# Kernel optimization log

Hardware: AMD Instinct MI355X
Metric: run time of the kernel (lower is better)

Reference implementation:

```python
import math
import jax, jax.numpy as jnp
import numpy as np

NUM_HEADS = 8
K_CRITICAL = 0.05
K_SKIP = 0.10


def setup_inputs() -> dict:
    key = jax.random.key(0)
    ks = jax.random.split(key, 10)
    B, T, D = 1, 2048, 512
    s = 1.0 / math.sqrt(D)
    return {
        'x': jax.random.normal(ks[0], (B, T, D), jnp.float32),
        'wq': jax.random.normal(ks[1], (D, D), jnp.float32) * s,
        'bq': jax.random.normal(ks[2], (D,), jnp.float32) * s,
        'wk': jax.random.normal(ks[3], (D, D), jnp.float32) * s,
        'bk': jax.random.normal(ks[4], (D,), jnp.float32) * s,
        'wv': jax.random.normal(ks[5], (D, D), jnp.float32) * s,
        'bv': jax.random.normal(ks[6], (D,), jnp.float32) * s,
        'wo': jax.random.normal(ks[7], (D, D), jnp.float32) * s,
        'bo': jax.random.normal(ks[8], (D,), jnp.float32) * s,
    }


def _phi(t):
    # elu(t) + 1 -> positive feature map for linear attention
    return jax.nn.elu(t) + 1.0


def reference(x, wq, bq, wk, bk, wv, bv, wo, bo):
    B, T, D = x.shape
    H = NUM_HEADS
    hd = D // H

    # projections (torch nn.Linear: y = x @ W.T + b), split heads -> [B,H,T,hd]
    q = (x @ wq.T + bq).reshape(B, T, H, hd).transpose(0, 2, 1, 3)
    k = (x @ wk.T + bk).reshape(B, T, H, hd).transpose(0, 2, 1, 3)
    v = (x @ wv.T + bv).reshape(B, T, H, hd).transpose(0, 2, 1, 3)

    # full attention scores [B,H,T,T]
    scores = jnp.einsum('bhqd,bhkd->bhqk', q, k) / math.sqrt(hd)

    # per-query quantile thresholds (linear interpolation, like torch.quantile)
    crit_th = jnp.quantile(scores, 1.0 - K_CRITICAL, axis=-1, keepdims=True)
    skip_th = jnp.quantile(scores, K_SKIP, axis=-1, keepdims=True)
    crit_mask = scores > crit_th
    skip_mask = scores < skip_th
    marginal_mask = jnp.logical_not(crit_mask | skip_mask)

    # critical path: softmax over top-k_critical entries only
    crit_scores = jnp.where(crit_mask, scores, -jnp.inf)
    crit_attn = jax.nn.softmax(crit_scores, axis=-1)
    crit_attn = jnp.where(skip_mask, 0.0, crit_attn)
    crit_out = jnp.einsum('bhqk,bhkd->bhqd', crit_attn, v)

    # marginal path: causal (cumulative) linear attention
    q_f = _phi(q)
    k_f = _phi(k)
    kv_cum = jnp.cumsum(k_f[..., :, None] * v[..., None, :], axis=2)  # [B,H,T,hd,hd]
    k_cum = jnp.cumsum(k_f, axis=2)                                   # [B,H,T,hd]
    lin_num = jnp.einsum('bhtd,bhtde->bhte', q_f, kv_cum)             # [B,H,T,hd]
    lin_den = jnp.clip(jnp.sum(q_f * k_cum, axis=-1, keepdims=True), 1e-6, None)
    marginal_active = jnp.mean(marginal_mask.astype(scores.dtype), axis=-1, keepdims=True)
    lin_out = (lin_num / lin_den) * marginal_active

    out = (crit_out + lin_out).transpose(0, 2, 1, 3).reshape(B, T, D)
    out = out @ wo.T + bo  # dropout is identity in eval mode
    return out
```

## Files before the change

kernel.cpp:

```cpp
#include <hip/hip_runtime.h>
#include <math.h>

#define T_SEQ 2048
#define D_MODEL 512
#define H_HEADS 8
#define HD 64
#define NCH 32
#define CSZ 64
#define CAP 192

__device__ __forceinline__ unsigned f2k(float f) {
    unsigned u = __float_as_uint(f);
    return (u & 0x80000000u) ? ~u : (u | 0x80000000u);
}
__device__ __forceinline__ float k2f(unsigned k) {
    unsigned u = (k & 0x80000000u) ? (k & 0x7fffffffu) : ~k;
    return __uint_as_float(u);
}

__device__ __forceinline__ void locate_rank(unsigned rr, unsigned e0,
    const unsigned cc[4], int lane, unsigned& sel_bin, unsigned& sel_nb, unsigned& sel_cnt)
{
    unsigned e1 = e0 + cc[0], e2 = e1 + cc[1], e3 = e2 + cc[2];
    int bin = -1; unsigned nb = 0u, ct = 0u;
    if (rr >= e0 && rr < e1)              { bin = lane * 4 + 0; nb = e0; ct = cc[0]; }
    else if (rr >= e1 && rr < e2)         { bin = lane * 4 + 1; nb = e1; ct = cc[1]; }
    else if (rr >= e2 && rr < e3)         { bin = lane * 4 + 2; nb = e2; ct = cc[2]; }
    else if (rr >= e3 && rr < e3 + cc[3]) { bin = lane * 4 + 3; nb = e3; ct = cc[3]; }
    unsigned long long bal = __ballot(bin >= 0);
    int src = __ffsll((unsigned long long)bal) - 1;
    sel_bin = (unsigned)__shfl(bin, src);
    sel_nb  = (unsigned)__shfl((int)nb, src);
    sel_cnt = (unsigned)__shfl((int)ct, src);
}

__global__ __launch_bounds__(256) void proj_qkv_kernel(
    const float* __restrict__ x,
    const float* __restrict__ wq, const float* __restrict__ bq,
    const float* __restrict__ wk, const float* __restrict__ bk,
    const float* __restrict__ wv, const float* __restrict__ bv,
    float* __restrict__ qh, float* __restrict__ kh, float* __restrict__ vh,
    float* __restrict__ qf, float* __restrict__ kf)
{
    const int which = blockIdx.z;
    const float* W    = (which == 0) ? wq : (which == 1) ? wk : wv;
    const float* bias = (which == 0) ? bq : (which == 1) ? bk : bv;
    float* outh = (which == 0) ? qh : (which == 1) ? kh : vh;
    float* outf = (which == 0) ? qf : (which == 1) ? kf : nullptr;

    __shared__ float As[32][68];
    __shared__ float Bs[32][68];
    const int tid = threadIdx.x;
    const int m0 = blockIdx.x * 64;
    const int n0 = blockIdx.y * 64;
    const int rb = (tid >> 4) * 4;
    const int cb = (tid & 15) * 4;

    float acc[4][4] = {};
    for (int k0 = 0; k0 < D_MODEL; k0 += 32) {
        for (int l = 0; l < 2; ++l) {
            int p = tid + l * 256;
            int row = p >> 3;
            int c4 = (p & 7) * 4;
            float4 av = *(const float4*)(x + (size_t)(m0 + row) * D_MODEL + k0 + c4);
            As[c4 + 0][row] = av.x; As[c4 + 1][row] = av.y;
            As[c4 + 2][row] = av.z; As[c4 + 3][row] = av.w;
            float4 wv4 = *(const float4*)(W + (size_t)(n0 + row) * D_MODEL + k0 + c4);
            Bs[c4 + 0][row] = wv4.x; Bs[c4 + 1][row] = wv4.y;
            Bs[c4 + 2][row] = wv4.z; Bs[c4 + 3][row] = wv4.w;
        }
        __syncthreads();
        #pragma unroll
        for (int kk = 0; kk < 32; ++kk) {
            float4 ar = *(const float4*)&As[kk][rb];
            float4 br = *(const float4*)&Bs[kk][cb];
            float arr[4] = {ar.x, ar.y, ar.z, ar.w};
            float brr[4] = {br.x, br.y, br.z, br.w};
            #pragma unroll
            for (int i = 0; i < 4; ++i)
                #pragma unroll
                for (int j = 0; j < 4; ++j)
                    acc[i][j] = fmaf(arr[i], brr[j], acc[i][j]);
        }
        __syncthreads();
    }
    #pragma unroll
    for (int i = 0; i < 4; ++i) {
        int m = m0 + rb + i;
        #pragma unroll
        for (int j = 0; j < 4; ++j) {
            int n = n0 + cb + j;
            float v = acc[i][j] + bias[n];
            int h = n >> 6, d = n & 63;
            size_t idx = ((size_t)(h * T_SEQ) + m) * HD + d;
            outh[idx] = v;
            if (outf) outf[idx] = (v > 0.f) ? (v + 1.f) : expf(v);
        }
    }
}

__global__ __launch_bounds__(256) void out_proj_kernel(
    const float* __restrict__ att, const float* __restrict__ wo,
    const float* __restrict__ bo, float* __restrict__ out)
{
    __shared__ float As[32][68];
    __shared__ float Bs[32][68];
    const int tid = threadIdx.x;
    const int m0 = blockIdx.x * 64;
    const int n0 = blockIdx.y * 64;
    const int rb = (tid >> 4) * 4;
    const int cb = (tid & 15) * 4;

    float acc[4][4] = {};
    for (int k0 = 0; k0 < D_MODEL; k0 += 32) {
        for (int l = 0; l < 2; ++l) {
            int p = tid + l * 256;
            int row = p >> 3;
            int c4 = (p & 7) * 4;
            float4 av = *(const float4*)(att + (size_t)(m0 + row) * D_MODEL + k0 + c4);
            As[c4 + 0][row] = av.x; As[c4 + 1][row] = av.y;
            As[c4 + 2][row] = av.z; As[c4 + 3][row] = av.w;
            float4 wv4 = *(const float4*)(wo + (size_t)(n0 + row) * D_MODEL + k0 + c4);
            Bs[c4 + 0][row] = wv4.x; Bs[c4 + 1][row] = wv4.y;
            Bs[c4 + 2][row] = wv4.z; Bs[c4 + 3][row] = wv4.w;
        }
        __syncthreads();
        #pragma unroll
        for (int kk = 0; kk < 32; ++kk) {
            float4 ar = *(const float4*)&As[kk][rb];
            float4 br = *(const float4*)&Bs[kk][cb];
            float arr[4] = {ar.x, ar.y, ar.z, ar.w};
            float brr[4] = {br.x, br.y, br.z, br.w};
            #pragma unroll
            for (int i = 0; i < 4; ++i)
                #pragma unroll
                for (int j = 0; j < 4; ++j)
                    acc[i][j] = fmaf(arr[i], brr[j], acc[i][j]);
        }
        __syncthreads();
    }
    #pragma unroll
    for (int i = 0; i < 4; ++i) {
        int m = m0 + rb + i;
        #pragma unroll
        for (int j = 0; j < 4; ++j) {
            int n = n0 + cb + j;
            out[(size_t)m * D_MODEL + n] = acc[i][j] + bo[n];
        }
    }
}

__global__ __launch_bounds__(256) void qk_gemm_kernel(
    const float* __restrict__ qh, const float* __restrict__ kh, float* __restrict__ S)
{
    __shared__ float As[64][132];
    __shared__ float Bs[64][68];
    const int tid = threadIdx.x;
    const int n0 = blockIdx.x * 64;
    const int m0 = blockIdx.y * 128;
    const int h  = blockIdx.z;
    const float* qb = qh + (size_t)h * T_SEQ * HD;
    const float* kb = kh + (size_t)h * T_SEQ * HD;

    #pragma unroll
    for (int l = 0; l < 8; ++l) {
        int p = tid + l * 256;
        int row = p >> 4, c4 = (p & 15) * 4;
        float4 a = *(const float4*)(qb + (size_t)(m0 + row) * HD + c4);
        As[c4 + 0][row] = a.x; As[c4 + 1][row] = a.y;
        As[c4 + 2][row] = a.z; As[c4 + 3][row] = a.w;
    }
    #pragma unroll
    for (int l = 0; l < 4; ++l) {
        int p = tid + l * 256;
        int row = p >> 4, c4 = (p & 15) * 4;
        float4 b = *(const float4*)(kb + (size_t)(n0 + row) * HD + c4);
        Bs[c4 + 0][row] = b.x; Bs[c4 + 1][row] = b.y;
        Bs[c4 + 2][row] = b.z; Bs[c4 + 3][row] = b.w;
    }
    __syncthreads();

    const int rb = (tid >> 4) * 8;
    const int cb = (tid & 15) * 4;
    float acc[8][4] = {};
    #pragma unroll 8
    for (int kk = 0; kk < HD; ++kk) {
        float4 a0 = *(const float4*)&As[kk][rb];
        float4 a1 = *(const float4*)&As[kk][rb + 4];
        float4 br = *(const float4*)&Bs[kk][cb];
        float arr[8] = {a0.x, a0.y, a0.z, a0.w, a1.x, a1.y, a1.z, a1.w};
        float brr[4] = {br.x, br.y, br.z, br.w};
        #pragma unroll
        for (int i = 0; i < 8; ++i)
            #pragma unroll
            for (int j = 0; j < 4; ++j)
                acc[i][j] = fmaf(arr[i], brr[j], acc[i][j]);
    }
    #pragma unroll
    for (int i = 0; i < 8; ++i) {
        float4 o;
        o.x = acc[i][0] * 0.125f; o.y = acc[i][1] * 0.125f;
        o.z = acc[i][2] * 0.125f; o.w = acc[i][3] * 0.125f;
        *(float4*)(S + ((size_t)h * T_SEQ + m0 + rb + i) * T_SEQ + n0 + cb) = o;
    }
}

__global__ __launch_bounds__(256) void select_kernel(
    const float* __restrict__ S, const float* __restrict__ vh,
    float* __restrict__ att, float* __restrict__ marg)
{
    const int h = blockIdx.y;
    const int r = threadIdx.x >> 6;
    const int lane = threadIdx.x & 63;
    const int t = blockIdx.x * 4 + r;
    __shared__ unsigned hists[4][2][256];

    const float* srow = S + ((size_t)h * T_SEQ + t) * T_SEQ;
    unsigned kr[32];
    unsigned mx = 0u;
    #pragma unroll
    for (int u = 0; u < 8; ++u) {
        float4 f = *(const float4*)(srow + (size_t)(lane + u * 64) * 4);
        kr[u * 4 + 0] = f2k(f.x); kr[u * 4 + 1] = f2k(f.y);
        kr[u * 4 + 2] = f2k(f.z); kr[u * 4 + 3] = f2k(f.w);
        mx = max(mx, max(max(kr[u * 4 + 0], kr[u * 4 + 1]), max(kr[u * 4 + 2], kr[u * 4 + 3])));
    }
    #pragma unroll
    for (int off = 32; off > 0; off >>= 1)
        mx = max(mx, (unsigned)__shfl_xor(mx, off));

    const unsigned rankv[2] = {204u, 1944u};
    unsigned pfx[2], base[2] = {0u, 0u}, fct[2] = {0u, 0u};
    bool res[2] = {false, false};
    unsigned rsh[2] = {0u, 0u};

    {
        uint4 z4 = make_uint4(0u, 0u, 0u, 0u);
        uint4* hv = (uint4*)hists[r];
        hv[lane * 2 + 0] = z4; hv[lane * 2 + 1] = z4;
        #pragma unroll
        for (int u = 0; u < 32; ++u)
            atomicAdd(&hists[r][0][kr[u] >> 24], 1u);
        uint4 a = ((const uint4*)hists[r][0])[lane];
        unsigned cc[4] = {a.x, a.y, a.z, a.w};
        unsigned lsum = cc[0] + cc[1] + cc[2] + cc[3];
        unsigned incl = lsum;
        #pragma unroll
        for (int off = 1; off < 64; off <<= 1) {
            unsigned tv = __shfl_up(incl, off);
            if (lane >= off) incl += tv;
        }
        unsigned e0 = incl - lsum;
        #pragma unroll
        for (int g = 0; g < 2; ++g) {
            unsigned bin, nb, ct;
            locate_rank(rankv[g], e0, cc, lane, bin, nb, ct);
            pfx[g] = bin; base[g] = nb; fct[g] = ct;
            if (ct == 1u) { res[g] = true; rsh[g] = 24u; }
        }
    }

    for (int p = 1; p < 4; ++p) {
        if (res[0] && res[1]) break;
        const int sh = 24 - 8 * p;
        const bool a0 = !res[0], a1 = !res[1];
        const bool dup = a0 && a1 && (pfx[0] == pfx[1]);
        uint4 z4 = make_uint4(0u, 0u, 0u, 0u);
        uint4* hv = (uint4*)hists[r];
        hv[lane * 2 + 0] = z4; hv[lane * 2 + 1] = z4;
        #pragma unroll
        for (int u = 0; u < 32; ++u) {
            unsigned k = kr[u];
            unsigned hi = k >> (sh + 8);
            unsigned bin = (k >> sh) & 255u;
            if (a0 && hi == pfx[0]) atomicAdd(&hists[r][0][bin], 1u);
            if (a1 && !dup && hi == pfx[1]) atomicAdd(&hists[r][1][bin], 1u);
        }
        unsigned cc0[4], e00 = 0u;
        if (a0 || dup) {
            uint4 a = ((const uint4*)hists[r][0])[lane];
            cc0[0] = a.x; cc0[1] = a.y; cc0[2] = a.z; cc0[3] = a.w;
            unsigned lsum = cc0[0] + cc0[1] + cc0[2] + cc0[3];
            unsigned incl = lsum;
            #pragma unroll
            for (int off = 1; off < 64; off <<= 1) {
                unsigned tv = __shfl_up(incl, off);
                if (lane >= off) incl += tv;
            }
            e00 = incl - lsum;
        }
        if (a0) {
            unsigned bin, nb, ct;
            locate_rank(rankv[0] - base[0], e00, cc0, lane, bin, nb, ct);
            pfx[0] = (pfx[0] << 8) | bin; base[0] += nb; fct[0] = ct;
            if (ct == 1u && p < 3) { res[0] = true; rsh[0] = (unsigned)sh; }
        }
        if (a1) {
            unsigned bin, nb, ct;
            if (dup) {
                locate_rank(rankv[1] - base[1], e00, cc0, lane, bin, nb, ct);
            } else {
                uint4 b = ((const uint4*)hists[r][1])[lane];
                unsigned cc1[4] = {b.x, b.y, b.z, b.w};
                unsigned lsum = cc1[0] + cc1[1] + cc1[2] + cc1[3];
                unsigned incl = lsum;
                #pragma unroll
                for (int off = 1; off < 64; off <<= 1) {
                    unsigned tv = __shfl_up(incl, off);
                    if (lane >= off) incl += tv;
                }
                unsigned e10 = incl - lsum;
                locate_rank(rankv[1] - base[1], e10, cc1, lane, bin, nb, ct);
            }
            pfx[1] = (pfx[1] << 8) | bin; base[1] += nb; fct[1] = ct;
            if (ct == 1u && p < 3) { res[1] = true; rsh[1] = (unsigned)sh; }
        }
    }

    unsigned kth0, kth1;
    if (res[0] || res[1]) {
        unsigned m0v = 0xffffffffu, m1v = 0xffffffffu;
        #pragma unroll
        for (int u = 0; u < 32; ++u) {
            unsigned k = kr[u];
            if (res[0] && (k >> rsh[0]) == pfx[0]) m0v = min(m0v, k);
            if (res[1] && (k >> rsh[1]) == pfx[1]) m1v = min(m1v, k);
        }
        #pragma unroll
        for (int off = 32; off > 0; off >>= 1) {
            m0v = min(m0v, (unsigned)__shfl_xor(m0v, off));
            m1v = min(m1v, (unsigned)__shfl_xor(m1v, off));
        }
        kth0 = res[0] ? m0v : pfx[0];
        kth1 = res[1] ? m1v : pfx[1];
    } else {
        kth0 = pfx[0]; kth1 = pfx[1];
    }
    (void)kth0;

    const unsigned cle0 = base[0] + fct[0];
    const unsigned scnt = (cle0 > 205u) ? base[0] : cle0;
    const float m = k2f(mx);

    float2* list = (float2*)hists[r];
    float z = 0.f;
    unsigned bcnt = 0;
    const unsigned long long pm = (lane == 0) ? 0ull : (~0ull >> (64 - lane));
    #pragma unroll
    for (int u8 = 0; u8 < 8; ++u8) {
        #pragma unroll
        for (int q = 0; q < 4; ++q) {
            unsigned k = kr[u8 * 4 + q];
            bool crit = k > kth1;
            unsigned long long bal = __ballot(crit);
            if (crit) {
                float sv = k2f(k);
                float w = __expf(sv - m);
                z += w;
                unsigned pos = bcnt + (unsigned)__popcll(bal & pm);
                if (pos < CAP) {
                    unsigned j = (unsigned)(4 * lane + 256 * u8 + q);
                    list[pos] = make_float2(w, __uint_as_float(j));
                }
            }
            bcnt += (unsigned)__popcll(bal);
        }
    }
    #pragma unroll
    for (int off = 32; off > 0; off >>= 1)
        z += __shfl_xor(z, off);
    const float invz = (z > 0.f) ? (1.f / z) : 0.f;

    const float* vb = vh + (size_t)h * T_SEQ * HD;
    const int cnt = (int)min(bcnt, (unsigned)CAP);
    float acc = 0.f;
    int i = 0;
    for (; i + 4 <= cnt; i += 4) {
        float2 e0 = list[i], e1 = list[i + 1], e2 = list[i + 2], e3 = list[i + 3];
        acc = fmaf(e0.x, vb[(size_t)__float_as_uint(e0.y) * HD + lane], acc);
        acc = fmaf(e1.x, vb[(size_t)__float_as_uint(e1.y) * HD + lane], acc);
        acc = fmaf(e2.x, vb[(size_t)__float_as_uint(e2.y) * HD + lane], acc);
        acc = fmaf(e3.x, vb[(size_t)__float_as_uint(e3.y) * HD + lane], acc);
    }
    for (; i < cnt; ++i) {
        float2 e = list[i];
        acc = fmaf(e.x, vb[(size_t)__float_as_uint(e.y) * HD + lane], acc);
    }
    att[(size_t)t * D_MODEL + h * HD + lane] = acc * invz;
    if (lane == 0) {
        unsigned mc = (unsigned)T_SEQ - bcnt - scnt;
        marg[(size_t)h * T_SEQ + t] = (float)mc * (1.f / (float)T_SEQ);
    }
}

__global__ __launch_bounds__(256) void chunk_sums_kernel(
    const float* __restrict__ kf, const float* __restrict__ vh,
    float* __restrict__ Ac, float* __restrict__ bc)
{
    const int c = blockIdx.x, h = blockIdx.y;
    const int tid = threadIdx.x;
    __shared__ float kfl[CSZ][HD];
    __shared__ float vl[CSZ][HD];
    const size_t base = ((size_t)h * T_SEQ + c * CSZ) * HD;

    for (int l = 0; l < 4; ++l) {
        int p = tid + l * 256;
        int row = p >> 4, c4 = (p & 15) * 4;
        *(float4*)&kfl[row][c4] = *(const float4*)(kf + base + (size_t)row * HD + c4);
        *(float4*)&vl[row][c4]  = *(const float4*)(vh + base + (size_t)row * HD + c4);
    }
    __syncthreads();

    const int d = tid >> 2, e0 = (tid & 3) * 16;
    float acc[16] = {};
    for (int u = 0; u < CSZ; ++u) {
        float a = kfl[u][d];
        #pragma unroll
        for (int i = 0; i < 16; ++i) acc[i] = fmaf(a, vl[u][e0 + i], acc[i]);
    }
    float* Adst = Ac + (((size_t)(h * NCH + c) * HD + d) * HD + e0);
    #pragma unroll
    for (int i = 0; i < 16; ++i) Adst[i] = acc[i];

    if (tid < HD) {
        float sum = 0.f;
        for (int u = 0; u < CSZ; ++u) sum += kfl[u][tid];
        bc[(size_t)(h * NCH + c) * HD + tid] = sum;
    }
}

__global__ __launch_bounds__(256) void prefix_kernel(
    const float* __restrict__ Ac, const float* __restrict__ bc,
    float* __restrict__ Sx, float* __restrict__ sx)
{
    const int h = blockIdx.x;
    const int tid = threadIdx.x;
    float run[16];
    #pragma unroll
    for (int i = 0; i < 16; ++i) run[i] = 0.f;
    for (int c = 0; c < NCH; ++c) {
        const float* a = Ac + (size_t)(h * NCH + c) * 4096;
        float* sdst = Sx + (size_t)(h * NCH + c) * 4096;
        #pragma unroll
        for (int i = 0; i < 16; ++i) {
            int idx = tid + i * 256;
            sdst[idx] = run[i];
            run[i] += a[idx];
        }
    }
    if (tid < HD) {
        float rb = 0.f;
        for (int c = 0; c < NCH; ++c) {
            sx[(size_t)(h * NCH + c) * HD + tid] = rb;
            rb += bc[(size_t)(h * NCH + c) * HD + tid];
        }
    }
}

__global__ __launch_bounds__(256) void lin_combine_kernel(
    const float* __restrict__ qf, const float* __restrict__ kf, const float* __restrict__ vh,
    const float* __restrict__ Sx, const float* __restrict__ sx,
    const float* __restrict__ marg, float* __restrict__ att)
{
    const int c = blockIdx.x, h = blockIdx.y;
    const int tid = threadIdx.x;
    __shared__ float Qs[CSZ][65];
    __shared__ float Ks[CSZ][65];
    __shared__ float P[CSZ][66];
    __shared__ float svv[HD];
    __shared__ float coef[CSZ];

    const size_t base = ((size_t)h * T_SEQ + c * CSZ) * HD;
    for (int l = 0; l < 4; ++l) {
        int p = tid + l * 256;
        int row = p >> 4, c4 = (p & 15) * 4;
        *(float4*)&Qs[row][c4] = *(const float4*)(qf + base + (size_t)row * HD + c4);
        *(float4*)&Ks[row][c4] = *(const float4*)(kf + base + (size_t)row * HD + c4);
    }
    if (tid < HD) svv[tid] = sx[(size_t)(h * NCH + c) * HD + tid];
    __syncthreads();

    {
        const int tq = tid >> 2, u0 = (tid & 3) * 16;
        float pr[16];
        #pragma unroll
        for (int i = 0; i < 16; ++i) pr[i] = 0.f;
        for (int d = 0; d < HD; ++d) {
            float qv = Qs[tq][d];
            #pragma unroll
            for (int i = 0; i < 16; ++i) pr[i] = fmaf(qv, Ks[u0 + i][d], pr[i]);
        }
        #pragma unroll
        for (int i = 0; i < 16; ++i) P[tq][u0 + i] = (u0 + i <= tq) ? pr[i] : 0.f;
    }
    __syncthreads();

    if (tid < CSZ) {
        const int tq = tid;
        float den = 0.f;
        for (int d = 0; d < HD; ++d) den += Qs[tq][d] * svv[d];
        for (int u = 0; u <= tq; ++u) den += P[tq][u];
        den = fmaxf(den, 1e-6f);
        coef[tq] = marg[(size_t)h * T_SEQ + c * CSZ + tq] / den;
    }
    {
        const float* Sbase = Sx + (size_t)(h * NCH + c) * 4096;
        for (int l = 0; l < 4; ++l) {
            int p = tid + l * 256;
            int row = p >> 4, c4 = (p & 15) * 4;
            *(float4*)&Ks[row][c4] = *(const float4*)(Sbase + (size_t)row * HD + c4);
        }
    }
    __syncthreads();

    {
        const int tq = tid >> 2, e0 = (tid & 3) * 16;
        float acc[16];
        #pragma unroll
        for (int i = 0; i < 16; ++i) acc[i] = 0.f;
        for (int d = 0; d < HD; ++d) {
            float qv = Qs[tq][d];
            #pragma unroll
            for (int i = 0; i < 16; ++i) acc[i] = fmaf(qv, Ks[d][e0 + i], acc[i]);
        }
        const float* vb = vh + base;
        for (int u = 0; u <= tq; ++u) {
            float pv = P[tq][u];
            #pragma unroll
            for (int i = 0; i < 16; ++i) acc[i] = fmaf(pv, vb[(size_t)u * HD + e0 + i], acc[i]);
        }
        const float cf = coef[tq];
        float* dst = att + (size_t)(c * CSZ + tq) * D_MODEL + h * HD + e0;
        #pragma unroll
        for (int i = 0; i < 16; ++i) dst[i] += acc[i] * cf;
    }
}

extern "C" void kernel_launch(void* const* d_in, const int* in_sizes, int n_in,
                              void* d_out, int out_size, void* d_ws, size_t ws_size,
                              hipStream_t stream)
{
    const float* x  = (const float*)d_in[0];
    const float* wq = (const float*)d_in[1];
    const float* bq = (const float*)d_in[2];
    const float* wk = (const float*)d_in[3];
    const float* bk = (const float*)d_in[4];
    const float* wv = (const float*)d_in[5];
    const float* bv = (const float*)d_in[6];
    const float* wo = (const float*)d_in[7];
    const float* bo = (const float*)d_in[8];
    float* out = (float*)d_out;

    float* ws = (float*)d_ws;
    const size_t NTD = (size_t)T_SEQ * D_MODEL;
    const size_t NSS = (size_t)H_HEADS * T_SEQ * T_SEQ;
    float* S    = ws;
    float* qh   = S + NSS;
    float* kh   = qh + NTD;
    float* vh   = kh + NTD;
    float* qf   = vh + NTD;
    float* kf   = qf + NTD;
    float* att  = kf + NTD;
    float* Ac   = att + NTD;
    float* Sx   = Ac + NTD;
    float* bc   = Sx + NTD;
    float* sx   = bc + 16384;
    float* marg = sx + 16384;

    dim3 b256(256);
    proj_qkv_kernel<<<dim3(32, 8, 3), b256, 0, stream>>>(x, wq, bq, wk, bk, wv, bv,
                                                         qh, kh, vh, qf, kf);
    qk_gemm_kernel<<<dim3(32, 16, 8), b256, 0, stream>>>(qh, kh, S);
    select_kernel<<<dim3(T_SEQ / 4, H_HEADS), b256, 0, stream>>>(S, vh, att, marg);
    chunk_sums_kernel<<<dim3(NCH, H_HEADS), b256, 0, stream>>>(kf, vh, Ac, bc);
    prefix_kernel<<<dim3(H_HEADS), b256, 0, stream>>>(Ac, bc, Sx, sx);
    lin_combine_kernel<<<dim3(NCH, H_HEADS), b256, 0, stream>>>(qf, kf, vh, Sx, sx, marg, att);
    out_proj_kernel<<<dim3(32, 8), b256, 0, stream>>>(att, wo, bo, out);
}
```

Measured before the change: 298.2 us.

## Fuse chunk prefix sums into lin_combine and drop exact kth refinement pass

```diff
diff --git a/kernel.cpp b/kernel.cpp
--- a/kernel.cpp
+++ b/kernel.cpp
@@ -229,10 +229,9 @@
     for (int off = 32; off > 0; off >>= 1)
         mx = max(mx, (unsigned)__shfl_xor(mx, off));
 
-    const unsigned rankv[2] = {204u, 1944u};
-    unsigned pfx[2], base[2] = {0u, 0u}, fct[2] = {0u, 0u};
-    bool res[2] = {false, false};
-    unsigned rsh[2] = {0u, 0u};
+    unsigned pfx0, pfx1, base0 = 0u, base1 = 0u, fct0 = 0u;
+    bool res0 = false, res1 = false;
+    unsigned rsh1 = 0u;
 
     {
         uint4 z4 = make_uint4(0u, 0u, 0u, 0u);
@@ -251,20 +250,20 @@
             if (lane >= off) incl += tv;
         }
         unsigned e0 = incl - lsum;
-        #pragma unroll
-        for (int g = 0; g < 2; ++g) {
-            unsigned bin, nb, ct;
-            locate_rank(rankv[g], e0, cc, lane, bin, nb, ct);
-            pfx[g] = bin; base[g] = nb; fct[g] = ct;
-            if (ct == 1u) { res[g] = true; rsh[g] = 24u; }
-        }
+        unsigned bin, nb, ct;
+        locate_rank(204u, e0, cc, lane, bin, nb, ct);
+        pfx0 = bin; base0 = nb; fct0 = ct;
+        if (ct == 1u) res0 = true;
+        locate_rank(1944u, e0, cc, lane, bin, nb, ct);
+        pfx1 = bin; base1 = nb;
+        if (ct == 1u) { res1 = true; rsh1 = 24u; }
     }
 
     for (int p = 1; p < 4; ++p) {
-        if (res[0] && res[1]) break;
+        if (res0 && res1) break;
         const int sh = 24 - 8 * p;
-        const bool a0 = !res[0], a1 = !res[1];
-        const bool dup = a0 && a1 && (pfx[0] == pfx[1]);
+        const bool a0 = !res0, a1 = !res1;
+        const bool dup = a0 && a1 && (pfx0 == pfx1);
         uint4 z4 = make_uint4(0u, 0u, 0u, 0u);
         uint4* hv = (uint4*)hists[r];
         hv[lane * 2 + 0] = z4; hv[lane * 2 + 1] = z4;
@@ -273,8 +272,8 @@
             unsigned k = kr[u];
             unsigned hi = k >> (sh + 8);
             unsigned bin = (k >> sh) & 255u;
-            if (a0 && hi == pfx[0]) atomicAdd(&hists[r][0][bin], 1u);
-            if (a1 && !dup && hi == pfx[1]) atomicAdd(&hists[r][1][bin], 1u);
+            if (a0 && hi == pfx0) atomicAdd(&hists[r][0][bin], 1u);
+            if (a1 && !dup && hi == pfx1) atomicAdd(&hists[r][1][bin], 1u);
         }
         unsigned cc0[4], e00 = 0u;
         if (a0 || dup) {
@@ -291,14 +290,14 @@
         }
         if (a0) {
             unsigned bin, nb, ct;
-            locate_rank(rankv[0] - base[0], e00, cc0, lane, bin, nb, ct);
-            pfx[0] = (pfx[0] << 8) | bin; base[0] += nb; fct[0] = ct;
-            if (ct == 1u && p < 3) { res[0] = true; rsh[0] = (unsigned)sh; }
+            locate_rank(204u - base0, e00, cc0, lane, bin, nb, ct);
+            pfx0 = (pfx0 << 8) | bin; base0 += nb; fct0 = ct;
+            if (ct == 1u && p < 3) res0 = true;
         }
         if (a1) {
             unsigned bin, nb, ct;
             if (dup) {
-                locate_rank(rankv[1] - base[1], e00, cc0, lane, bin, nb, ct);
+                locate_rank(1944u - base1, e00, cc0, lane, bin, nb, ct);
             } else {
                 uint4 b = ((const uint4*)hists[r][1])[lane];
                 unsigned cc1[4] = {b.x, b.y, b.z, b.w};
@@ -310,36 +309,15 @@
                     if (lane >= off) incl += tv;
                 }
                 unsigned e10 = incl - lsum;
-                locate_rank(rankv[1] - base[1], e10, cc1, lane, bin, nb, ct);
+                locate_rank(1944u - base1, e10, cc1, lane, bin, nb, ct);
             }
-            pfx[1] = (pfx[1] << 8) | bin; base[1] += nb; fct[1] = ct;
-            if (ct == 1u && p < 3) { res[1] = true; rsh[1] = (unsigned)sh; }
-        }
-    }
-
-    unsigned kth0, kth1;
-    if (res[0] || res[1]) {
-        unsigned m0v = 0xffffffffu, m1v = 0xffffffffu;
-        #pragma unroll
-        for (int u = 0; u < 32; ++u) {
-            unsigned k = kr[u];
-            if (res[0] && (k >> rsh[0]) == pfx[0]) m0v = min(m0v, k);
-            if (res[1] && (k >> rsh[1]) == pfx[1]) m1v = min(m1v, k);
-        }
-        #pragma unroll
-        for (int off = 32; off > 0; off >>= 1) {
-            m0v = min(m0v, (unsigned)__shfl_xor(m0v, off));
-            m1v = min(m1v, (unsigned)__shfl_xor(m1v, off));
-        }
-        kth0 = res[0] ? m0v : pfx[0];
-        kth1 = res[1] ? m1v : pfx[1];
-    } else {
-        kth0 = pfx[0]; kth1 = pfx[1];
-    }
-    (void)kth0;
-
-    const unsigned cle0 = base[0] + fct[0];
-    const unsigned scnt = (cle0 > 205u) ? base[0] : cle0;
+            pfx1 = (pfx1 << 8) | bin; base1 += nb;
+            if (ct == 1u && p < 3) { res1 = true; rsh1 = (unsigned)sh; }
+        }
+    }
+
+    const unsigned cle0 = base0 + fct0;
+    const unsigned scnt = (cle0 > 205u) ? base0 : cle0;
     const float m = k2f(mx);
 
     float2* list = (float2*)hists[r];
@@ -351,7 +329,7 @@
         #pragma unroll
         for (int q = 0; q < 4; ++q) {
             unsigned k = kr[u8 * 4 + q];
-            bool crit = k > kth1;
+            bool crit = (k >> rsh1) > pfx1;
             unsigned long long bal = __ballot(crit);
             if (crit) {
                 float sv = k2f(k);
@@ -429,37 +407,9 @@
     }
 }
 
-__global__ __launch_bounds__(256) void prefix_kernel(
-    const float* __restrict__ Ac, const float* __restrict__ bc,
-    float* __restrict__ Sx, float* __restrict__ sx)
-{
-    const int h = blockIdx.x;
-    const int tid = threadIdx.x;
-    float run[16];
-    #pragma unroll
-    for (int i = 0; i < 16; ++i) run[i] = 0.f;
-    for (int c = 0; c < NCH; ++c) {
-        const float* a = Ac + (size_t)(h * NCH + c) * 4096;
-        float* sdst = Sx + (size_t)(h * NCH + c) * 4096;
-        #pragma unroll
-        for (int i = 0; i < 16; ++i) {
-            int idx = tid + i * 256;
-            sdst[idx] = run[i];
-            run[i] += a[idx];
-        }
-    }
-    if (tid < HD) {
-        float rb = 0.f;
-        for (int c = 0; c < NCH; ++c) {
-            sx[(size_t)(h * NCH + c) * HD + tid] = rb;
-            rb += bc[(size_t)(h * NCH + c) * HD + tid];
-        }
-    }
-}
-
 __global__ __launch_bounds__(256) void lin_combine_kernel(
     const float* __restrict__ qf, const float* __restrict__ kf, const float* __restrict__ vh,
-    const float* __restrict__ Sx, const float* __restrict__ sx,
+    const float* __restrict__ Ac, const float* __restrict__ bc,
     const float* __restrict__ marg, float* __restrict__ att)
 {
     const int c = blockIdx.x, h = blockIdx.y;
@@ -477,7 +427,23 @@
         *(float4*)&Qs[row][c4] = *(const float4*)(qf + base + (size_t)row * HD + c4);
         *(float4*)&Ks[row][c4] = *(const float4*)(kf + base + (size_t)row * HD + c4);
     }
-    if (tid < HD) svv[tid] = sx[(size_t)(h * NCH + c) * HD + tid];
+
+    float4 sA[4];
+    #pragma unroll
+    for (int l = 0; l < 4; ++l) sA[l] = make_float4(0.f, 0.f, 0.f, 0.f);
+    float sb = 0.f;
+    {
+        const float* Abase = Ac + (size_t)(h * NCH) * 4096;
+        for (int cc = 0; cc < c; ++cc) {
+            const float* a = Abase + (size_t)cc * 4096;
+            #pragma unroll
+            for (int l = 0; l < 4; ++l) {
+                float4 v = *(const float4*)(a + 4 * (tid + l * 256));
+                sA[l].x += v.x; sA[l].y += v.y; sA[l].z += v.z; sA[l].w += v.w;
+            }
+            if (tid < HD) sb += bc[(size_t)(h * NCH + cc) * HD + tid];
+        }
+    }
     __syncthreads();
 
     {
@@ -495,6 +461,13 @@
     }
     __syncthreads();
 
+    #pragma unroll
+    for (int l = 0; l < 4; ++l) {
+        int p = tid + l * 256;
+        int row = p >> 4, c4 = (p & 15) * 4;
+        *(float4*)&Ks[row][c4] = sA[l];
+    }
+    if (tid < HD) svv[tid] = sb;
     if (tid < CSZ) {
         const int tq = tid;
         float den = 0.f;
@@ -502,14 +475,6 @@
         for (int u = 0; u <= tq; ++u) den += P[tq][u];
         den = fmaxf(den, 1e-6f);
         coef[tq] = marg[(size_t)h * T_SEQ + c * CSZ + tq] / den;
-    }
-    {
-        const float* Sbase = Sx + (size_t)(h * NCH + c) * 4096;
-        for (int l = 0; l < 4; ++l) {
-            int p = tid + l * 256;
-            int row = p >> 4, c4 = (p & 15) * 4;
-            *(float4*)&Ks[row][c4] = *(const float4*)(Sbase + (size_t)row * HD + c4);
-        }
     }
     __syncthreads();
 
@@ -562,10 +527,8 @@
     float* kf   = qf + NTD;
     float* att  = kf + NTD;
     float* Ac   = att + NTD;
-    float* Sx   = Ac + NTD;
-    float* bc   = Sx + NTD;
-    float* sx   = bc + 16384;
-    float* marg = sx + 16384;
+    float* bc   = Ac + NTD;
+    float* marg = bc + 16384;
 
     dim3 b256(256);
     proj_qkv_kernel<<<dim3(32, 8, 3), b256, 0, stream>>>(x, wq, bq, wk, bk, wv, bv,
@@ -573,7 +536,6 @@
     qk_gemm_kernel<<<dim3(32, 16, 8), b256, 0, stream>>>(qh, kh, S);
     select_kernel<<<dim3(T_SEQ / 4, H_HEADS), b256, 0, stream>>>(S, vh, att, marg);
     chunk_sums_kernel<<<dim3(NCH, H_HEADS), b256, 0, stream>>>(kf, vh, Ac, bc);
-    prefix_kernel<<<dim3(H_HEADS), b256, 0, stream>>>(Ac, bc, Sx, sx);
-    lin_combine_kernel<<<dim3(NCH, H_HEADS), b256, 0, stream>>>(qf, kf, vh, Sx, sx, marg, att);
+    lin_combine_kernel<<<dim3(NCH, H_HEADS), b256, 0, stream>>>(qf, kf, vh, Ac, bc, marg, att);
     out_proj_kernel<<<dim3(32, 8), b256, 0, stream>>>(att, wo, bo, out);
 }
```

New measurement: 287.5 us. -3.6%, faster.
